# Performance work log

Measured on AMD Instinct MI355X. Metric: run time of the kernel, lower is better.

## Reference

```python
import jax, jax.numpy as jnp
import numpy as np

B, S, H = 2, 2048, 1024
NH = 16
HD = H // NH  # 64


def setup_inputs() -> dict:
    key = jax.random.key(0)
    ks = jax.random.split(key, 12)
    s = 1.0 / np.sqrt(H)
    return {
        "x_q": jax.random.normal(ks[0], (B, S, H), jnp.float32),
        "x_k": jax.random.normal(ks[1], (B, S, H), jnp.float32),
        "x_v": jax.random.normal(ks[2], (B, S, H), jnp.float32),
        "attention_mask": jax.random.randint(ks[3], (B, S), 0, 2, jnp.int32),
        "Wq": jax.random.normal(ks[4], (H, H), jnp.float32) * s,
        "bq": jnp.zeros((H,), jnp.float32),
        "Wk": jax.random.normal(ks[5], (H, H), jnp.float32) * s,
        "bk": jnp.zeros((H,), jnp.float32),
        "Wv": jax.random.normal(ks[6], (H, H), jnp.float32) * s,
        "bv": jnp.zeros((H,), jnp.float32),
        "Wo": jax.random.normal(ks[7], (H, H), jnp.float32) * s,
        "bo": jnp.zeros((H,), jnp.float32),
    }


def reference(x_q, x_k, x_v, attention_mask, Wq, bq, Wk, bk, Wv, bv, Wo, bo):
    b, s, h = x_q.shape
    # projections
    q = x_q @ Wq + bq
    k = x_k @ Wk + bk
    v = x_v @ Wv + bv
    # [B, NH, S, HD]
    q = q.reshape(b, s, NH, HD).transpose(0, 2, 1, 3)
    k = k.reshape(b, s, NH, HD).transpose(0, 2, 1, 3)
    v = v.reshape(b, s, NH, HD).transpose(0, 2, 1, 3)
    scores = jnp.einsum("bhqd,bhkd->bhqk", q, k) / jnp.sqrt(jnp.float32(HD))
    # key-padding mask: 1 -> keep (0 bias), else -inf; broadcast [B,1,1,S]
    bias = jnp.where(attention_mask == 1, 0.0, -jnp.inf).astype(scores.dtype)
    scores = scores + bias[:, None, None, :]
    attn = jax.nn.softmax(scores, axis=-1)
    # dropout prob = 0.0 (eval / deterministic): identity
    out = jnp.einsum("bhqk,bhkd->bhqd", attn, v)
    out = out.transpose(0, 2, 1, 3).reshape(b, s, h)
    return out @ Wo + bo
```

## Files before the change

kernel.cpp:

```cpp
#include <hip/hip_runtime.h>

#define DEVI static __device__ __forceinline__

typedef unsigned short u16;
typedef unsigned int u32;
typedef __attribute__((ext_vector_type(8))) __bf16 bf16x8;
typedef __attribute__((ext_vector_type(8))) short short8;
typedef __attribute__((ext_vector_type(4))) float f32x4;
typedef __attribute__((ext_vector_type(16))) float f32x16;
typedef __attribute__((ext_vector_type(4))) u32 u32x4;

DEVI u16 f2bf(float f) {
  union { float f; u32 u; } v; v.f = f;
  u32 r = v.u + 0x7fffu + ((v.u >> 16) & 1u);
  return (u16)(r >> 16);
}

DEVI u16 bfc(float f) {
  union { __bf16 b; u16 u; } v; v.b = (__bf16)f; return v.u;
}

DEVI void gload16(const void* g, void* l) {
  __builtin_amdgcn_global_load_lds(
      (const __attribute__((address_space(1))) void*)g,
      (__attribute__((address_space(3))) void*)l,
      16, 0, 0);
}

__global__ void k_cvt3(const float* __restrict__ a, const float* __restrict__ b2,
                       const float* __restrict__ c, u16* __restrict__ out, int n4) {
  const int z = blockIdx.y;
  const float* in = (z == 0) ? a : ((z == 1) ? b2 : c);
  u16* o = out + (size_t)z * (size_t)n4 * 4;
  const int i = blockIdx.x * blockDim.x + threadIdx.x;
  if (i >= n4) return;
  const float4 v = reinterpret_cast<const float4*>(in)[i];
  ushort4 s;
  s.x = f2bf(v.x); s.y = f2bf(v.y); s.z = f2bf(v.z); s.w = f2bf(v.w);
  reinterpret_cast<ushort4*>(o)[i] = s;
}

__global__ void k_maskbias(const int* __restrict__ m, float* __restrict__ bias, int n) {
  int i = blockIdx.x * blockDim.x + threadIdx.x;
  if (i < n) bias[i] = (m[i] == 1) ? 0.f : -1e30f;
}

__global__ void k_transcvt4(const float* __restrict__ W0, const float* __restrict__ W1,
                            const float* __restrict__ W2, const float* __restrict__ W3,
                            u16* __restrict__ Wtb) {
  const int z = blockIdx.z;
  const float* W = (z == 0) ? W0 : ((z == 1) ? W1 : ((z == 2) ? W2 : W3));
  u16* Wt = Wtb + (size_t)z * 1024 * 1024;
  __shared__ float tl[32][33];
  const int n0 = blockIdx.x * 32, k0 = blockIdx.y * 32;
  const int tx = threadIdx.x, ty = threadIdx.y;
#pragma unroll
  for (int r = ty; r < 32; r += 8)
    tl[r][tx] = W[(size_t)(k0 + r) * 1024 + n0 + tx];
  __syncthreads();
#pragma unroll
  for (int r = ty; r < 32; r += 8)
    Wt[(size_t)(n0 + r) * 1024 + k0 + tx] = f2bf(tl[tx][r]);
}

DEVI void store1(u16* C, size_t i, float v) { C[i] = f2bf(v); }
DEVI void store1(float* C, size_t i, float v) { C[i] = v; }

template <typename OutT>
__global__ __launch_bounds__(256, 2) void k_gemm_bt(
    const u16* __restrict__ Abase, long aZ,
    const u16* __restrict__ Btbase, long bZ,
    const float* __restrict__ bias0, const float* __restrict__ bias1,
    const float* __restrict__ bias2,
    float s0, float s1, float s2,
    OutT* __restrict__ Cbase, long cZ, u16* __restrict__ Vt,
    int M, int N, int K) {
  const int z = blockIdx.z;
  const u16* A  = Abase  + (size_t)z * aZ;
  const u16* Bt = Btbase + (size_t)z * bZ;
  OutT* C = Cbase + (size_t)z * cZ;
  const float* bias = (z == 0) ? bias0 : ((z == 1) ? bias1 : bias2);
  const float scl = (z == 0) ? s0 : ((z == 1) ? s1 : s2);

  __shared__ u16 lsA[128 * 32];
  __shared__ u16 lsB[128 * 32];

  const int t = threadIdx.x;
  const int w = t >> 6, ln = t & 63;
  const int l15 = ln & 15, lhi = ln >> 4;
  const int wr = w >> 1, wc = w & 1;
  const int m0 = blockIdx.x * 128, n0 = blockIdx.y * 128;

  f32x4 acc[4][4] = {};

  for (int kt = 0; kt < K; kt += 32) {
#pragma unroll
    for (int i = 0; i < 2; ++i) {
      const int li = i * 256 + t;
      const int row = li >> 2, cb = (li & 3) << 3;
      gload16(A + (size_t)(m0 + row) * K + kt + cb,
              (char*)lsA + (i * 256 + w * 64) * 16);
      gload16(Bt + (size_t)(n0 + row) * K + kt + cb,
              (char*)lsB + (i * 256 + w * 64) * 16);
    }
    __syncthreads();

    bf16x8 af[4], bf_[4];
#pragma unroll
    for (int m = 0; m < 4; ++m)
      af[m] = *reinterpret_cast<const bf16x8*>(
          &lsA[(wr * 64 + m * 16 + l15) * 32 + lhi * 8]);
#pragma unroll
    for (int n = 0; n < 4; ++n)
      bf_[n] = *reinterpret_cast<const bf16x8*>(
          &lsB[(wc * 64 + n * 16 + l15) * 32 + lhi * 8]);
#pragma unroll
    for (int m = 0; m < 4; ++m)
#pragma unroll
      for (int n = 0; n < 4; ++n)
        acc[m][n] = __builtin_amdgcn_mfma_f32_16x16x32_bf16(af[m], bf_[n], acc[m][n], 0, 0, 0);
    __syncthreads();
  }

  if (Vt != nullptr && z == 2) {
#pragma unroll
    for (int n = 0; n < 4; ++n) {
      const int c = n0 + wc * 64 + n * 16 + l15;
      const float bv = bias[c];
#pragma unroll
      for (int m = 0; m < 4; ++m) {
        const int r = m0 + wr * 64 + m * 16 + lhi * 4;
        ushort4 s4;
#pragma unroll
        for (int j = 0; j < 4; ++j) ((u16*)&s4)[j] = f2bf(acc[m][n][j] + bv);
        *reinterpret_cast<ushort4*>(
            &Vt[((size_t)((r >> 11) * 1024 + c)) * 2048 + (r & 2047)]) = s4;
      }
    }
    return;
  }

#pragma unroll
  for (int n = 0; n < 4; ++n) {
    const int c = n0 + wc * 64 + n * 16 + l15;
    const float bv = bias[c];
#pragma unroll
    for (int m = 0; m < 4; ++m)
#pragma unroll
      for (int j = 0; j < 4; ++j) {
        const int r = m0 + wr * 64 + m * 16 + lhi * 4 + j;
        store1(C, (size_t)r * N + c, (acc[m][n][j] + bv) * scl);
      }
  }
}

__global__ __launch_bounds__(256, 2) void k_attn(
    const u16* __restrict__ Q, const u16* __restrict__ K, const u16* __restrict__ Vt,
    const float* __restrict__ MB, u16* __restrict__ O) {
  __shared__ u16 lsK[3][64][72];
  __shared__ u16 lsV[2][64][72];

  const int t = threadIdx.x, w = t >> 6, ln = t & 63;
  const int l31 = ln & 31, h = ln >> 5, h8 = h * 8;
  const int fid = blockIdx.x;
  const int xcd = fid & 7, slot = fid >> 3;
  const int pair = xcd * 4 + (slot >> 4);
  const int qt = slot & 15;
  const int hh = pair & 15, b = pair >> 4;

  const size_t rowQ = (size_t)b * 2048 + qt * 128 + w * 32;
  const int hc = hh * 64;

  const int srow = t >> 3, scol = (t & 7) << 3;
  const u16* Kg = K + ((size_t)b * 2048 + srow) * 1024 + hc + scol;
  const int half = t & 1;
  const int g16 = ((t & 7) >> 1) << 4;
  const u16* VgA = Vt + ((size_t)(b * 1024 + hc) + srow) * 2048 + g16 + 4 * half;
  const float* MBb = MB + b * 2048;

  bf16x8 qb[4];
#pragma unroll
  for (int ks = 0; ks < 4; ++ks)
    qb[ks] = *reinterpret_cast<const bf16x8*>(
        &Q[(rowQ + l31) * 1024 + hc + ks * 16 + h8]);

  f32x16 o[2];
#pragma unroll
  for (int i = 0; i < 16; ++i) { o[0][i] = 0.f; o[1][i] = 0.f; }
  float mrow = -1e30f, lsum = 0.f;

#pragma unroll
  for (int p = 0; p < 3; ++p) {
    const short8 a = *reinterpret_cast<const short8*>(Kg + (size_t)(p * 64) * 1024);
    const short8 c = *reinterpret_cast<const short8*>(Kg + (size_t)(p * 64 + 32) * 1024);
    *reinterpret_cast<short8*>(&lsK[p][srow][scol]) = a;
    *reinterpret_cast<short8*>(&lsK[p][32 + srow][scol]) = c;
  }
#pragma unroll
  for (int p = 0; p < 2; ++p) {
    const ushort4 a = *reinterpret_cast<const ushort4*>(VgA + p * 64);
    const ushort4 b4 = *reinterpret_cast<const ushort4*>(VgA + p * 64 + 8);
    const ushort4 c = *reinterpret_cast<const ushort4*>(VgA + 32 * 2048 + p * 64);
    const ushort4 d = *reinterpret_cast<const ushort4*>(VgA + 32 * 2048 + p * 64 + 8);
    *reinterpret_cast<ushort4*>(&lsV[p][srow][scol]) = a;
    *reinterpret_cast<ushort4*>(&lsV[p][srow][scol + 4]) = b4;
    *reinterpret_cast<ushort4*>(&lsV[p][32 + srow][scol]) = c;
    *reinterpret_cast<ushort4*>(&lsV[p][32 + srow][scol + 4]) = d;
  }
  __syncthreads();

  f32x16 stA[2], stB[2];
#pragma unroll
  for (int i = 0; i < 16; ++i) { stA[0][i] = 0.f; stA[1][i] = 0.f; }
#pragma unroll
  for (int ks = 0; ks < 4; ++ks) {
    const bf16x8 kb0 = *reinterpret_cast<const bf16x8*>(&lsK[0][l31][ks * 16 + h8]);
    const bf16x8 kb1 = *reinterpret_cast<const bf16x8*>(&lsK[0][32 + l31][ks * 16 + h8]);
    stA[0] = __builtin_amdgcn_mfma_f32_32x32x16_bf16(kb0, qb[ks], stA[0], 0, 0, 0);
    stA[1] = __builtin_amdgcn_mfma_f32_32x32x16_bf16(kb1, qb[ks], stA[1], 0, 0, 0);
  }

#define ATTN_BODY(T, CUR, NXT, SW)                                                  \
  {                                                                                 \
    const int tK = ((T) + 3) & 31, tV = ((T) + 2) & 31;                             \
    const short8 rk0 = *reinterpret_cast<const short8*>(Kg + (size_t)(tK * 64) * 1024); \
    const short8 rk1 = *reinterpret_cast<const short8*>(Kg + (size_t)(tK * 64 + 32) * 1024); \
    const ushort4 rv0a = *reinterpret_cast<const ushort4*>(VgA + tV * 64);          \
    const ushort4 rv0b = *reinterpret_cast<const ushort4*>(VgA + tV * 64 + 8);      \
    const ushort4 rv1a = *reinterpret_cast<const ushort4*>(VgA + 32 * 2048 + tV * 64); \
    const ushort4 rv1b = *reinterpret_cast<const ushort4*>(VgA + 32 * 2048 + tV * 64 + 8); \
    const int sK = ((SW) == 2) ? 0 : (SW) + 1;                                      \
    _Pragma("unroll")                                                               \
    for (int i = 0; i < 16; ++i) { NXT[0][i] = 0.f; NXT[1][i] = 0.f; }              \
    __builtin_amdgcn_s_setprio(1);                                                  \
    _Pragma("unroll")                                                               \
    for (int ks = 0; ks < 4; ++ks) {                                                \
      const bf16x8 kb0 = *reinterpret_cast<const bf16x8*>(&lsK[sK][l31][ks * 16 + h8]); \
      const bf16x8 kb1 = *reinterpret_cast<const bf16x8*>(&lsK[sK][32 + l31][ks * 16 + h8]); \
      NXT[0] = __builtin_amdgcn_mfma_f32_32x32x16_bf16(kb0, qb[ks], NXT[0], 0, 0, 0); \
      NXT[1] = __builtin_amdgcn_mfma_f32_32x32x16_bf16(kb1, qb[ks], NXT[1], 0, 0, 0); \
    }                                                                               \
    __builtin_amdgcn_s_setprio(0);                                                  \
    _Pragma("unroll")                                                               \
    for (int f = 0; f < 2; ++f)                                                     \
      _Pragma("unroll")                                                             \
      for (int rg = 0; rg < 4; ++rg) {                                              \
        const f32x4 bv = *reinterpret_cast<const f32x4*>(                           \
            &MBb[(T) * 64 + f * 32 + rg * 8 + h * 4]);                              \
        _Pragma("unroll")                                                           \
        for (int jj = 0; jj < 4; ++jj) CUR[f][rg * 4 + jj] += bv[jj];               \
      }                                                                             \
    float tm = CUR[0][0];                                                           \
    _Pragma("unroll")                                                               \
    for (int f = 0; f < 2; ++f)                                                     \
      _Pragma("unroll")                                                             \
      for (int i = 0; i < 16; ++i) tm = fmaxf(tm, CUR[f][i]);                       \
    tm = fmaxf(tm, __shfl_xor(tm, 32, 64));                                         \
    const bool trig = tm > mrow + 8.f;                                              \
    if (__any(trig)) {                                                              \
      const float al = trig ? __builtin_amdgcn_exp2f(mrow - tm) : 1.f;              \
      if (trig) mrow = tm;                                                          \
      lsum *= al;                                                                   \
      _Pragma("unroll")                                                             \
      for (int f = 0; f < 2; ++f)                                                   \
        _Pragma("unroll")                                                           \
        for (int i = 0; i < 16; ++i) o[f][i] *= al;                                 \
    }                                                                               \
    float rs = 0.f;                                                                 \
    _Pragma("unroll")                                                               \
    for (int f = 0; f < 2; ++f)                                                     \
      _Pragma("unroll")                                                             \
      for (int i = 0; i < 16; ++i) {                                                \
        const float p = __builtin_amdgcn_exp2f(CUR[f][i] - mrow);                   \
        CUR[f][i] = p;                                                              \
        rs += p;                                                                    \
      }                                                                             \
    rs += __shfl_xor(rs, 32, 64);                                                   \
    lsum += rs;                                                                     \
    __builtin_amdgcn_s_setprio(1);                                                  \
    _Pragma("unroll")                                                               \
    for (int f = 0; f < 2; ++f) {                                                   \
      u32 pk[8];                                                                    \
      _Pragma("unroll")                                                             \
      for (int i = 0; i < 8; ++i)                                                   \
        pk[i] = (u32)bfc(CUR[f][2 * i]) | ((u32)bfc(CUR[f][2 * i + 1]) << 16);      \
      _Pragma("unroll")                                                             \
      for (int s = 0; s < 2; ++s) {                                                 \
        u32x4 pw;                                                                   \
        pw[0] = pk[4 * s + 0]; pw[1] = pk[4 * s + 1];                               \
        pw[2] = pk[4 * s + 2]; pw[3] = pk[4 * s + 3];                               \
        const bf16x8 pb = __builtin_bit_cast(bf16x8, pw);                           \
        const int ks = f * 2 + s;                                                   \
        _Pragma("unroll")                                                           \
        for (int df2 = 0; df2 < 2; ++df2) {                                         \
          const bf16x8 vt = *reinterpret_cast<const bf16x8*>(                       \
              &lsV[(T) & 1][df2 * 32 + l31][ks * 16 + h8]);                         \
          o[df2] = __builtin_amdgcn_mfma_f32_32x32x16_bf16(vt, pb, o[df2], 0, 0, 0); \
        }                                                                           \
      }                                                                             \
    }                                                                               \
    __builtin_amdgcn_s_setprio(0);                                                  \
    __syncthreads();                                                                \
    *reinterpret_cast<short8*>(&lsK[SW][srow][scol]) = rk0;                         \
    *reinterpret_cast<short8*>(&lsK[SW][32 + srow][scol]) = rk1;                    \
    *reinterpret_cast<ushort4*>(&lsV[(T) & 1][srow][scol]) = rv0a;                  \
    *reinterpret_cast<ushort4*>(&lsV[(T) & 1][srow][scol + 4]) = rv0b;              \
    *reinterpret_cast<ushort4*>(&lsV[(T) & 1][32 + srow][scol]) = rv1a;             \
    *reinterpret_cast<ushort4*>(&lsV[(T) & 1][32 + srow][scol + 4]) = rv1b;         \
  }

  int sw = 0;
  for (int t2 = 0; t2 < 32; t2 += 2) {
    ATTN_BODY(t2, stA, stB, sw);
    sw = (sw == 2) ? 0 : sw + 1;
    ATTN_BODY(t2 + 1, stB, stA, sw);
    sw = (sw == 2) ? 0 : sw + 1;
  }
#undef ATTN_BODY

  const float inv = 1.f / lsum;
#pragma unroll
  for (int df2 = 0; df2 < 2; ++df2)
#pragma unroll
    for (int rg = 0; rg < 4; ++rg) {
      ushort4 s4;
      s4.x = bfc(o[df2][rg * 4 + 0] * inv);
      s4.y = bfc(o[df2][rg * 4 + 1] * inv);
      s4.z = bfc(o[df2][rg * 4 + 2] * inv);
      s4.w = bfc(o[df2][rg * 4 + 3] * inv);
      *reinterpret_cast<ushort4*>(
          &O[(rowQ + l31) * 1024 + hc + df2 * 32 + rg * 8 + h * 4]) = s4;
    }
}

extern "C" void kernel_launch(void* const* d_in, const int* in_sizes, int n_in,
                              void* d_out, int out_size, void* d_ws, size_t ws_size,
                              hipStream_t stream) {
  const float* x_q = (const float*)d_in[0];
  const float* x_k = (const float*)d_in[1];
  const float* x_v = (const float*)d_in[2];
  const int*   msk = (const int*)d_in[3];
  const float* Wq  = (const float*)d_in[4];
  const float* bq  = (const float*)d_in[5];
  const float* Wk  = (const float*)d_in[6];
  const float* bk  = (const float*)d_in[7];
  const float* Wv  = (const float*)d_in[8];
  const float* bv  = (const float*)d_in[9];
  const float* Wo  = (const float*)d_in[10];
  const float* bo  = (const float*)d_in[11];

  const size_t NTOK = 4096, H = 1024;
  u16* xbf  = (u16*)d_ws;
  u16* wt   = xbf + 3 * NTOK * H;
  u16* qkv  = wt  + 4 * H * H;
  u16* aout = qkv + 3 * NTOK * H;
  float* mb = (float*)(aout + NTOK * H);
  u16* vtb  = qkv + 2 * NTOK * H;

  k_cvt3<<<dim3(4096, 3), dim3(256), 0, stream>>>(x_q, x_k, x_v, xbf, 1048576);
  k_maskbias<<<dim3(16), dim3(256), 0, stream>>>(msk, mb, 4096);
  k_transcvt4<<<dim3(32, 32, 4), dim3(32, 8), 0, stream>>>(Wq, Wk, Wv, Wo, wt);

  const float qscale = 0.125f * 1.4426950408889634f;
  k_gemm_bt<u16><<<dim3(32, 8, 3), dim3(256), 0, stream>>>(
      xbf, (long)(NTOK * H), wt, (long)(H * H), bq, bk, bv,
      qscale, 1.f, 1.f,
      qkv, (long)(NTOK * H), vtb, 4096, 1024, 1024);

  k_attn<<<dim3(512), dim3(256), 0, stream>>>(
      qkv, qkv + NTOK * H, vtb, mb, aout);

  k_gemm_bt<float><<<dim3(32, 8, 1), dim3(256), 0, stream>>>(
      aout, 0L, wt + 3 * H * H, 0L, bo, bo, bo,
      1.f, 1.f, 1.f,
      (float*)d_out, 0L, nullptr, 4096, 1024, 1024);
}
```

Measured before the change: 149.2 us.

## Fuse fp32-to-bf16 input conversion into QKV GEMM and preload mask bias into score accumulators

After: 137.1 us. 1.09x faster.

```diff
diff --git a/kernel.cpp b/kernel.cpp
--- a/kernel.cpp
+++ b/kernel.cpp
@@ -25,19 +25,6 @@
       (const __attribute__((address_space(1))) void*)g,
       (__attribute__((address_space(3))) void*)l,
       16, 0, 0);
-}
-
-__global__ void k_cvt3(const float* __restrict__ a, const float* __restrict__ b2,
-                       const float* __restrict__ c, u16* __restrict__ out, int n4) {
-  const int z = blockIdx.y;
-  const float* in = (z == 0) ? a : ((z == 1) ? b2 : c);
-  u16* o = out + (size_t)z * (size_t)n4 * 4;
-  const int i = blockIdx.x * blockDim.x + threadIdx.x;
-  if (i >= n4) return;
-  const float4 v = reinterpret_cast<const float4*>(in)[i];
-  ushort4 s;
-  s.x = f2bf(v.x); s.y = f2bf(v.y); s.z = f2bf(v.z); s.w = f2bf(v.w);
-  reinterpret_cast<ushort4*>(o)[i] = s;
 }
 
 __global__ void k_maskbias(const int* __restrict__ m, float* __restrict__ bias, int n) {
@@ -66,9 +53,11 @@
 DEVI void store1(u16* C, size_t i, float v) { C[i] = f2bf(v); }
 DEVI void store1(float* C, size_t i, float v) { C[i] = v; }
 
-template <typename OutT>
+template <typename OutT, bool CVTA>
 __global__ __launch_bounds__(256, 2) void k_gemm_bt(
-    const u16* __restrict__ Abase, long aZ,
+    const u16* __restrict__ Ab, long aZ,
+    const float* __restrict__ Af0, const float* __restrict__ Af1,
+    const float* __restrict__ Af2,
     const u16* __restrict__ Btbase, long bZ,
     const float* __restrict__ bias0, const float* __restrict__ bias1,
     const float* __restrict__ bias2,
@@ -76,7 +65,8 @@
     OutT* __restrict__ Cbase, long cZ, u16* __restrict__ Vt,
     int M, int N, int K) {
   const int z = blockIdx.z;
-  const u16* A  = Abase  + (size_t)z * aZ;
+  const u16* A  = Ab + (size_t)z * aZ;
+  const float* Af = (z == 0) ? Af0 : ((z == 1) ? Af1 : Af2);
   const u16* Bt = Btbase + (size_t)z * bZ;
   OutT* C = Cbase + (size_t)z * cZ;
   const float* bias = (z == 0) ? bias0 : ((z == 1) ? bias1 : bias2);
@@ -98,8 +88,18 @@
     for (int i = 0; i < 2; ++i) {
       const int li = i * 256 + t;
       const int row = li >> 2, cb = (li & 3) << 3;
-      gload16(A + (size_t)(m0 + row) * K + kt + cb,
-              (char*)lsA + (i * 256 + w * 64) * 16);
+      if constexpr (CVTA) {
+        const float* ap = Af + (size_t)(m0 + row) * K + kt + cb;
+        const float4 f0 = *reinterpret_cast<const float4*>(ap);
+        const float4 f1 = *reinterpret_cast<const float4*>(ap + 4);
+        union { u16 us[8]; short8 s8; } u;
+        u.us[0] = bfc(f0.x); u.us[1] = bfc(f0.y); u.us[2] = bfc(f0.z); u.us[3] = bfc(f0.w);
+        u.us[4] = bfc(f1.x); u.us[5] = bfc(f1.y); u.us[6] = bfc(f1.z); u.us[7] = bfc(f1.w);
+        *reinterpret_cast<short8*>((char*)lsA + (size_t)li * 16) = u.s8;
+      } else {
+        gload16(A + (size_t)(m0 + row) * K + kt + cb,
+                (char*)lsA + (i * 256 + w * 64) * 16);
+      }
       gload16(Bt + (size_t)(n0 + row) * K + kt + cb,
               (char*)lsB + (i * 256 + w * 64) * 16);
     }
@@ -211,7 +211,13 @@
 
   f32x16 stA[2], stB[2];
 #pragma unroll
-  for (int i = 0; i < 16; ++i) { stA[0][i] = 0.f; stA[1][i] = 0.f; }
+  for (int f = 0; f < 2; ++f)
+#pragma unroll
+    for (int rg = 0; rg < 4; ++rg) {
+      const f32x4 bv = *reinterpret_cast<const f32x4*>(&MBb[f * 32 + rg * 8 + h * 4]);
+#pragma unroll
+      for (int jj = 0; jj < 4; ++jj) stA[f][rg * 4 + jj] = bv[jj];
+    }
 #pragma unroll
   for (int ks = 0; ks < 4; ++ks) {
     const bf16x8 kb0 = *reinterpret_cast<const bf16x8*>(&lsK[0][l31][ks * 16 + h8]);
@@ -222,7 +228,7 @@
 
 #define ATTN_BODY(T, CUR, NXT, SW)                                                  \
   {                                                                                 \
-    const int tK = ((T) + 3) & 31, tV = ((T) + 2) & 31;                             \
+    const int tK = ((T) + 3) & 31, tV = ((T) + 2) & 31, tB = ((T) + 1) & 31;        \
     const short8 rk0 = *reinterpret_cast<const short8*>(Kg + (size_t)(tK * 64) * 1024); \
     const short8 rk1 = *reinterpret_cast<const short8*>(Kg + (size_t)(tK * 64 + 32) * 1024); \
     const ushort4 rv0a = *reinterpret_cast<const ushort4*>(VgA + tV * 64);          \
@@ -231,7 +237,14 @@
     const ushort4 rv1b = *reinterpret_cast<const ushort4*>(VgA + 32 * 2048 + tV * 64 + 8); \
     const int sK = ((SW) == 2) ? 0 : (SW) + 1;                                      \
     _Pragma("unroll")                                                               \
-    for (int i = 0; i < 16; ++i) { NXT[0][i] = 0.f; NXT[1][i] = 0.f; }              \
+    for (int f = 0; f < 2; ++f)                                                     \
+      _Pragma("unroll")                                                             \
+      for (int rg = 0; rg < 4; ++rg) {                                              \
+        const f32x4 bv = *reinterpret_cast<const f32x4*>(                           \
+            &MBb[tB * 64 + f * 32 + rg * 8 + h * 4]);                               \
+        _Pragma("unroll")                                                           \
+        for (int jj = 0; jj < 4; ++jj) NXT[f][rg * 4 + jj] = bv[jj];                \
+      }                                                                             \
     __builtin_amdgcn_s_setprio(1);                                                  \
     _Pragma("unroll")                                                               \
     for (int ks = 0; ks < 4; ++ks) {                                                \
@@ -241,15 +254,6 @@
       NXT[1] = __builtin_amdgcn_mfma_f32_32x32x16_bf16(kb1, qb[ks], NXT[1], 0, 0, 0); \
     }                                                                               \
     __builtin_amdgcn_s_setprio(0);                                                  \
-    _Pragma("unroll")                                                               \
-    for (int f = 0; f < 2; ++f)                                                     \
-      _Pragma("unroll")                                                             \
-      for (int rg = 0; rg < 4; ++rg) {                                              \
-        const f32x4 bv = *reinterpret_cast<const f32x4*>(                           \
-            &MBb[(T) * 64 + f * 32 + rg * 8 + h * 4]);                              \
-        _Pragma("unroll")                                                           \
-        for (int jj = 0; jj < 4; ++jj) CUR[f][rg * 4 + jj] += bv[jj];               \
-      }                                                                             \
     float tm = CUR[0][0];                                                           \
     _Pragma("unroll")                                                               \
     for (int f = 0; f < 2; ++f)                                                     \
@@ -350,28 +354,26 @@
   const float* bo  = (const float*)d_in[11];
 
   const size_t NTOK = 4096, H = 1024;
-  u16* xbf  = (u16*)d_ws;
-  u16* wt   = xbf + 3 * NTOK * H;
+  u16* wt   = (u16*)d_ws;
   u16* qkv  = wt  + 4 * H * H;
   u16* aout = qkv + 3 * NTOK * H;
   float* mb = (float*)(aout + NTOK * H);
   u16* vtb  = qkv + 2 * NTOK * H;
 
-  k_cvt3<<<dim3(4096, 3), dim3(256), 0, stream>>>(x_q, x_k, x_v, xbf, 1048576);
   k_maskbias<<<dim3(16), dim3(256), 0, stream>>>(msk, mb, 4096);
   k_transcvt4<<<dim3(32, 32, 4), dim3(32, 8), 0, stream>>>(Wq, Wk, Wv, Wo, wt);
 
   const float qscale = 0.125f * 1.4426950408889634f;
-  k_gemm_bt<u16><<<dim3(32, 8, 3), dim3(256), 0, stream>>>(
-      xbf, (long)(NTOK * H), wt, (long)(H * H), bq, bk, bv,
+  k_gemm_bt<u16, true><<<dim3(32, 8, 3), dim3(256), 0, stream>>>(
+      nullptr, 0L, x_q, x_k, x_v, wt, (long)(H * H), bq, bk, bv,
       qscale, 1.f, 1.f,
       qkv, (long)(NTOK * H), vtb, 4096, 1024, 1024);
 
   k_attn<<<dim3(512), dim3(256), 0, stream>>>(
       qkv, qkv + NTOK * H, vtb, mb, aout);
 
-  k_gemm_bt<float><<<dim3(32, 8, 1), dim3(256), 0, stream>>>(
-      aout, 0L, wt + 3 * H * H, 0L, bo, bo, bo,
+  k_gemm_bt<float, false><<<dim3(32, 8, 1), dim3(256), 0, stream>>>(
+      aout, 0L, nullptr, nullptr, nullptr, wt + 3 * H * H, 0L, bo, bo, bo,
       1.f, 1.f, 1.f,
       (float*)d_out, 0L, nullptr, 4096, 1024, 1024);
 }
```
